# Kernel tuning notes

Hardware: AMD Instinct MI355X
Metric: run time of the kernel (lower is better)

## Reference

```python
import jax, jax.numpy as jnp
import numpy as np

T, BSZ, IDIM, CDIM, NH, N, M = 128, 256, 256, 512, 1, 128, 64


def _address(mem, k, beta, g, s, gamma, w_prev):
    # preproc (matches NTMMemory._preproc)
    beta = jax.nn.softplus(beta)          # [b,1]
    g = jax.nn.sigmoid(g)                 # [b,1]
    s = jax.nn.softmax(s, axis=1)         # [b,3]
    gamma = 1.0 + jax.nn.softplus(gamma)  # [b,1]
    # content addressing: cosine similarity (eps=1e-8 norm clamp as in torch)
    mm = mem + 1e-16                      # [b,N,M]
    kk = k[:, None, :] + 1e-16            # [b,1,M]
    dot = jnp.sum(mm * kk, axis=-1)       # [b,N]
    nm = jnp.maximum(jnp.linalg.norm(mm, axis=-1), 1e-8)
    nk = jnp.maximum(jnp.linalg.norm(kk, axis=-1), 1e-8)
    wc = jax.nn.softmax(beta * (dot / (nm * nk)), axis=1)
    # interpolate
    wg = g * wc + (1.0 - g) * w_prev
    # circular 3-tap shift (modulo convolve): out[i] = s0*w[i-1] + s1*w[i] + s2*w[i+1]
    ww = (s[:, 0:1] * jnp.roll(wg, 1, axis=1)
          + s[:, 1:2] * wg
          + s[:, 2:3] * jnp.roll(wg, -1, axis=1))
    # sharpen
    w = ww ** gamma
    return w / (jnp.sum(w, axis=1, keepdims=True) + 1e-16)


def _split_head(o, m):
    return (o[:, :m], o[:, m:m + 1], o[:, m + 1:m + 2], o[:, m + 2:m + 5], o[:, m + 5:m + 6])


def _forward(inp, hid, c0, mem_bias, r0, W_ih, W_hh, b_ih, b_hh, read_W, read_b, write_W, write_b):
    Tt, bsz, _ = inp.shape
    num_heads = read_W.shape[0]
    n, m = mem_bias.shape
    cdim = c0.shape[0]

    h = hid[0]                                              # [b, cdim]
    c = jnp.broadcast_to(c0, (bsz, cdim))
    mem = jnp.broadcast_to(mem_bias, (bsz, n, m))           # [b, N, M]
    reads = jnp.broadcast_to(r0[:, None, :], (num_heads, bsz, m))
    w_states = jnp.zeros((2 * num_heads, bsz, n), inp.dtype)

    def step(carry, emb):
        h, c, mem, reads, w_states = carry
        x = jnp.concatenate([emb] + [reads[i] for i in range(num_heads)], axis=1)
        gates = x @ W_ih.T + h @ W_hh.T + b_ih + b_hh
        gi, gf, gg, go = jnp.split(gates, 4, axis=1)
        c = jax.nn.sigmoid(gf) * c + jax.nn.sigmoid(gi) * jnp.tanh(gg)
        h = jax.nn.sigmoid(go) * jnp.tanh(c)
        new_reads, new_ws = [], []
        for hi in range(num_heads):
            # read head
            o = h @ read_W[hi] + read_b[hi]                 # [b, M+6]
            k, beta, g, s, gamma = _split_head(o, m)
            w = _address(mem, k, beta, g, s, gamma, w_states[2 * hi])
            new_reads.append(jnp.einsum('bn,bnm->bm', w, mem))
            new_ws.append(w)
            # write head
            o = h @ write_W[hi] + write_b[hi]               # [b, 3M+6]
            k, beta, g, s, gamma = _split_head(o, m)
            e = jax.nn.sigmoid(o[:, m + 6:2 * m + 6])
            a = o[:, 2 * m + 6:3 * m + 6]
            w = _address(mem, k, beta, g, s, gamma, w_states[2 * hi + 1])
            mem = mem * (1.0 - w[:, :, None] * e[:, None, :]) + w[:, :, None] * a[:, None, :]
            new_ws.append(w)
        reads = jnp.stack(new_reads)
        w_states = jnp.stack(new_ws)
        out = jnp.concatenate([h] + new_reads, axis=1)      # [b, cdim + NH*M]
        return (h, c, mem, reads, w_states), out

    _, os = jax.lax.scan(step, (h, c, mem, reads, w_states), inp)
    return os                                               # [T, b, cdim + NH*M]


def setup_inputs() -> dict:
    key = jax.random.key(0)
    ks = jax.random.split(key, 10)
    lstm_std = 5.0 / np.sqrt(IDIM + M * NH + CDIM)
    mem_std = 1.0 / np.sqrt(N + M)
    return {
        'inp': jax.random.normal(ks[0], (T, BSZ, IDIM), jnp.float32),
        'hid': jax.random.normal(ks[1], (1, BSZ, CDIM), jnp.float32) * 0.05,
        'c0': jax.random.normal(ks[2], (CDIM,), jnp.float32) * 0.05,
        'mem_bias': jax.random.uniform(ks[3], (N, M), jnp.float32, -mem_std, mem_std),
        'r0': jax.random.normal(ks[4], (NH, M), jnp.float32) * 0.02,
        'W_ih': jax.random.uniform(ks[5], (4 * CDIM, IDIM + M * NH), jnp.float32, -lstm_std, lstm_std),
        'W_hh': jax.random.uniform(ks[6], (4 * CDIM, CDIM), jnp.float32, -lstm_std, lstm_std),
        'b_ih': jnp.zeros((4 * CDIM,), jnp.float32),
        'b_hh': jnp.zeros((4 * CDIM,), jnp.float32),
        'read_W': jax.random.normal(ks[7], (NH, CDIM, M + 6), jnp.float32) * 0.05,
        'read_b': jnp.zeros((NH, M + 6), jnp.float32),
        'write_W': jax.random.normal(ks[8], (NH, CDIM, 3 * M + 6), jnp.float32) * 0.05,
        'write_b': jnp.zeros((NH, 3 * M + 6), jnp.float32),
    }


def reference(inp, hid, c0, mem_bias, r0, W_ih, W_hh, b_ih, b_hh, read_W, read_b, write_W, write_b):
    return _forward(inp, hid, c0, mem_bias, r0, W_ih, W_hh, b_ih, b_hh,
                    read_W, read_b, write_W, write_b)
```

## Files before the change

kernel.cpp:

```cpp
#include <hip/hip_runtime.h>
#include <math.h>

#define TT   128
#define BSZ  256
#define IDIM 256
#define CDIM 512
#define NN   128
#define MM   64
#define KTOT 832
#define GJ   2048
#define ODIM 576
#define OC   268

#define NKB1 26
#define NJT1 32
#define NKB2 16
#define NJT2 17

typedef __attribute__((ext_vector_type(8))) short s16x8;
typedef __attribute__((ext_vector_type(4))) float f32x4;
#define MFMA __builtin_amdgcn_mfma_f32_16x16x32_bf16

__device__ __forceinline__ float sigmoidf_(float x) { return 1.0f / (1.0f + expf(-x)); }
__device__ __forceinline__ float softplusf_(float x) {
    return (x > 0.f) ? (x + log1pf(expf(-x))) : log1pf(expf(x));
}
__device__ __forceinline__ unsigned short f2bf(float f) {
    unsigned int u = __builtin_bit_cast(unsigned int, f);
    u += 0x7FFFu + ((u >> 16) & 1u);
    return (unsigned short)(u >> 16);
}
__device__ __forceinline__ float bf2f(unsigned short b) {
    unsigned int u = ((unsigned int)b) << 16;
    return __builtin_bit_cast(float, u);
}
__device__ __forceinline__ void split2(float v, unsigned short& h, unsigned short& lo) {
    h = f2bf(v);
    lo = f2bf(v - bf2f(h));
}

__global__ void k_packB1(const float* __restrict__ W_ih, const float* __restrict__ W_hh,
                         const float* __restrict__ b_ih, const float* __restrict__ b_hh,
                         unsigned short* __restrict__ Bh, unsigned short* __restrict__ Bl,
                         float* __restrict__ bias)
{
    const int total = NKB1 * NJT1 * 4 * 64 * 8;
    for (int idx = blockIdx.x * 256 + threadIdx.x; idx < total + GJ; idx += gridDim.x * 256) {
        if (idx < total) {
            int e  = idx & 7;
            int l  = (idx >> 3) & 63;
            int g  = (idx >> 9) & 3;
            int jt = (idx >> 11) & 31;
            int kb = idx >> 16;
            int k  = kb * 32 + ((l >> 4) << 3) + e;
            int n  = g * 512 + jt * 16 + (l & 15);
            float v = (k < 320) ? W_ih[n * 320 + k] : W_hh[n * 512 + (k - 320)];
            unsigned short h_, l_;
            split2(v, h_, l_);
            Bh[idx] = h_; Bl[idx] = l_;
        } else {
            int j = idx - total;
            bias[j] = b_ih[j] + b_hh[j];
        }
    }
}

__global__ void k_packB2(const float* __restrict__ rW, const float* __restrict__ rb,
                         const float* __restrict__ wW, const float* __restrict__ wb,
                         unsigned short* __restrict__ Bh, unsigned short* __restrict__ Bl,
                         float* __restrict__ bias2)
{
    const int total = NKB2 * NJT2 * 64 * 8;
    for (int idx = blockIdx.x * 256 + threadIdx.x; idx < total + NJT2 * 16; idx += gridDim.x * 256) {
        if (idx < total) {
            int e   = idx & 7;
            int l   = (idx >> 3) & 63;
            int q   = idx >> 9;
            int jt  = q % 17;
            int kb  = q / 17;
            int k   = kb * 32 + ((l >> 4) << 3) + e;
            int col = jt * 16 + (l & 15);
            float v = 0.f;
            if (col < 70)       v = rW[k * 70 + col];
            else if (col < OC)  v = wW[k * 198 + (col - 70)];
            unsigned short h_, l_;
            split2(v, h_, l_);
            Bh[idx] = h_; Bl[idx] = l_;
        } else {
            int col = idx - total;
            bias2[col] = (col < 70) ? rb[col] : ((col < OC) ? wb[col - 70] : 0.f);
        }
    }
}

__global__ void k_init(const float* __restrict__ hid, const float* __restrict__ c0,
                       const float* __restrict__ mem_bias, const float* __restrict__ r0,
                       float* __restrict__ h0, float* __restrict__ cst, float* __restrict__ mem,
                       float* __restrict__ rdv, float* __restrict__ w_r, float* __restrict__ w_w)
{
    const int A = BSZ * CDIM;
    const int B = A + BSZ * CDIM;
    const int C = B + BSZ * NN * MM;
    const int D = C + BSZ * MM;
    const int E = D + 2 * BSZ * NN;
    for (int idx = blockIdx.x * 256 + threadIdx.x; idx < E; idx += gridDim.x * 256) {
        if (idx < A) h0[idx] = hid[idx];
        else if (idx < B) { int i = idx - A; cst[i] = c0[i & (CDIM - 1)]; }
        else if (idx < C) { int i = idx - B; mem[i] = mem_bias[i & (NN * MM - 1)]; }
        else if (idx < D) { int i = idx - C; rdv[i] = r0[i & (MM - 1)]; }
        else { int i = idx - D; if (i < BSZ * NN) w_r[i] = 0.f; else w_w[i - BSZ * NN] = 0.f; }
    }
}

__global__ __launch_bounds__(256) void k_gates_mfma(
    const float* __restrict__ x_emb, const float* __restrict__ read_v,
    const float* __restrict__ h_in,
    const unsigned short* __restrict__ Bh, const unsigned short* __restrict__ Bl,
    const float* __restrict__ bias,
    float* __restrict__ c_st, float* __restrict__ h_out, float* __restrict__ out_t)
{
    __shared__ __align__(16) unsigned short AH[4][32][40];
    __shared__ __align__(16) unsigned short AL[4][32][40];
    __shared__ float red[4][32][4][16];
    const int tid = threadIdx.x;
    const int w = tid >> 6, l = tid & 63;
    const int jt = blockIdx.x;
    const int m0 = blockIdx.y * 32;

    f32x4 acc[2][4];
#pragma unroll
    for (int s = 0; s < 2; ++s)
#pragma unroll
        for (int g = 0; g < 4; ++g) acc[s][g] = (f32x4){0.f, 0.f, 0.f, 0.f};

    const int row_s = l >> 1;
    const int c0 = (l & 1) * 16;
    const int rr = l & 15;
    const int kq = (l >> 4) * 8;

    for (int i = 0; i < 7; ++i) {
        const int kb = i * 4 + w;
        const bool act = (kb < NKB1);
        s16x8 bfh[4], bfl[4];
        if (act) {
            const int boff = ((kb * 32 + jt) * 256 + l) * 8;
#pragma unroll
            for (int g = 0; g < 4; ++g) {
                bfh[g] = *(const s16x8*)(Bh + boff + g * 512);
                bfl[g] = *(const s16x8*)(Bl + boff + g * 512);
            }
            const int kg = kb * 32;
            const float* p;
            if (kb < 8)       p = x_emb + (m0 + row_s) * IDIM + kg + c0;
            else if (kb < 10) p = read_v + (m0 + row_s) * MM + (kg - IDIM) + c0;
            else              p = h_in + (m0 + row_s) * CDIM + (kg - 320) + c0;
            float f[16];
            *(float4*)&f[0]  = ((const float4*)p)[0];
            *(float4*)&f[4]  = ((const float4*)p)[1];
            *(float4*)&f[8]  = ((const float4*)p)[2];
            *(float4*)&f[12] = ((const float4*)p)[3];
            s16x8 vh0, vl0, vh1, vl1;
#pragma unroll
            for (int q = 0; q < 8; ++q) {
                unsigned short h_, l_;
                split2(f[q], h_, l_);
                vh0[q] = (short)h_; vl0[q] = (short)l_;
                split2(f[8 + q], h_, l_);
                vh1[q] = (short)h_; vl1[q] = (short)l_;
            }
            *(s16x8*)&AH[w][row_s][c0]     = vh0;
            *(s16x8*)&AH[w][row_s][c0 + 8] = vh1;
            *(s16x8*)&AL[w][row_s][c0]     = vl0;
            *(s16x8*)&AL[w][row_s][c0 + 8] = vl1;
        }
        __syncthreads();
        if (act) {
            s16x8 a0h = *(const s16x8*)&AH[w][rr][kq];
            s16x8 a0l = *(const s16x8*)&AL[w][rr][kq];
            s16x8 a1h = *(const s16x8*)&AH[w][16 + rr][kq];
            s16x8 a1l = *(const s16x8*)&AL[w][16 + rr][kq];
#pragma unroll
            for (int g = 0; g < 4; ++g) {
                acc[0][g] = MFMA(a0h, bfh[g], acc[0][g], 0, 0, 0);
                acc[1][g] = MFMA(a1h, bfh[g], acc[1][g], 0, 0, 0);
                acc[0][g] = MFMA(a0l, bfh[g], acc[0][g], 0, 0, 0);
                acc[1][g] = MFMA(a1l, bfh[g], acc[1][g], 0, 0, 0);
                acc[0][g] = MFMA(a0h, bfl[g], acc[0][g], 0, 0, 0);
                acc[1][g] = MFMA(a1h, bfl[g], acc[1][g], 0, 0, 0);
            }
        }
        __syncthreads();
    }

#pragma unroll
    for (int s = 0; s < 2; ++s)
#pragma unroll
        for (int g = 0; g < 4; ++g)
#pragma unroll
            for (int r = 0; r < 4; ++r)
                red[w][s * 16 + (l >> 4) * 4 + r][g][l & 15] = acc[s][g][r];
    __syncthreads();
    const int j = tid & 15, r0 = tid >> 4;
#pragma unroll
    for (int s = 0; s < 2; ++s) {
        const int row = s * 16 + r0;
        const int b = m0 + row;
        const int jg = jt * 16 + j;
        float gv0 = red[0][row][0][j] + red[1][row][0][j] + red[2][row][0][j] + red[3][row][0][j];
        float gv1 = red[0][row][1][j] + red[1][row][1][j] + red[2][row][1][j] + red[3][row][1][j];
        float gv2 = red[0][row][2][j] + red[1][row][2][j] + red[2][row][2][j] + red[3][row][2][j];
        float gv3 = red[0][row][3][j] + red[1][row][3][j] + red[2][row][3][j] + red[3][row][3][j];
        float gi = gv0 + bias[jg];
        float gf = gv1 + bias[512 + jg];
        float gg = gv2 + bias[1024 + jg];
        float go = gv3 + bias[1536 + jg];
        float cn = sigmoidf_(gf) * c_st[b * CDIM + jg] + sigmoidf_(gi) * tanhf(gg);
        float hn = sigmoidf_(go) * tanhf(cn);
        c_st[b * CDIM + jg] = cn;
        h_out[b * CDIM + jg] = hn;
        out_t[b * ODIM + jg] = hn;
    }
}

__global__ __launch_bounds__(256) void k_heads_mfma(
    const float* __restrict__ h,
    const unsigned short* __restrict__ Bh, const unsigned short* __restrict__ Bl,
    const float* __restrict__ bias2, float* __restrict__ o_all)
{
    __shared__ __align__(16) unsigned short AH[4][16][40];
    __shared__ __align__(16) unsigned short AL[4][16][40];
    __shared__ float red[4][16][16];
    const int tid = threadIdx.x;
    const int w = tid >> 6, l = tid & 63;
    const int jt = blockIdx.x;
    const int m0 = blockIdx.y * 16;

    f32x4 acc = (f32x4){0.f, 0.f, 0.f, 0.f};
    const int row_s = l >> 2;
    const int c0 = (l & 3) * 8;
    const int rr = l & 15;
    const int kq = (l >> 4) * 8;

    for (int i = 0; i < 4; ++i) {
        const int kb = i * 4 + w;
        const int boff = ((kb * NJT2 + jt) * 64 + l) * 8;
        s16x8 bh = *(const s16x8*)(Bh + boff);
        s16x8 bl = *(const s16x8*)(Bl + boff);
        const float* p = h + (m0 + row_s) * CDIM + kb * 32 + c0;
        float f[8];
        *(float4*)&f[0] = ((const float4*)p)[0];
        *(float4*)&f[4] = ((const float4*)p)[1];
        s16x8 vh, vl;
#pragma unroll
        for (int q = 0; q < 8; ++q) {
            unsigned short h_, l_;
            split2(f[q], h_, l_);
            vh[q] = (short)h_; vl[q] = (short)l_;
        }
        *(s16x8*)&AH[w][row_s][c0] = vh;
        *(s16x8*)&AL[w][row_s][c0] = vl;
        __syncthreads();
        s16x8 ah = *(const s16x8*)&AH[w][rr][kq];
        s16x8 al = *(const s16x8*)&AL[w][rr][kq];
        acc = MFMA(ah, bh, acc, 0, 0, 0);
        acc = MFMA(al, bh, acc, 0, 0, 0);
        acc = MFMA(ah, bl, acc, 0, 0, 0);
        __syncthreads();
    }
#pragma unroll
    for (int r = 0; r < 4; ++r)
        red[w][(l >> 4) * 4 + r][l & 15] = acc[r];
    __syncthreads();
    const int j = tid & 15, row = tid >> 4;
    const int col = jt * 16 + j;
    if (col < OC) {
        float o = red[0][row][j] + red[1][row][j] + red[2][row][j] + red[3][row][j] + bias2[col];
        o_all[(m0 + row) * OC + col] = o;
    }
}

__global__ __launch_bounds__(256) void k_address(
    const float* __restrict__ o_all,
    float* __restrict__ mem,
    float* __restrict__ rdv,
    float* __restrict__ w_r,
    float* __restrict__ w_w,
    float* __restrict__ out_t)
{
    const int b = blockIdx.x, tid = threadIdx.x;
    __shared__ float ms[NN * 65];
    __shared__ float os[OC];
    __shared__ float wgs[NN];
    __shared__ float wsh[NN];
    __shared__ float red4[4];
    __shared__ float esh[MM], ash[MM];

    for (int i = tid; i < NN * MM / 4; i += 256) {
        int n = i >> 4, m4 = (i & 15) * 4;
        float4 v = *(const float4*)&mem[(size_t)b * NN * MM + n * MM + m4];
        ms[n * 65 + m4 + 0] = v.x;
        ms[n * 65 + m4 + 1] = v.y;
        ms[n * 65 + m4 + 2] = v.z;
        ms[n * 65 + m4 + 3] = v.w;
    }
    for (int i = tid; i < OC; i += 256) os[i] = o_all[b * OC + i];
    __syncthreads();

    for (int head = 0; head < 2; ++head) {
        const int ob = head ? 70 : 0;
        const float* wprev = head ? w_w : w_r;
        float* wstore = head ? w_w : w_r;

        float beta  = softplusf_(os[ob + 64]);
        float g     = sigmoidf_(os[ob + 65]);
        float s0r = os[ob + 66], s1r = os[ob + 67], s2r = os[ob + 68];
        float smx = fmaxf(s0r, fmaxf(s1r, s2r));
        float e0 = expf(s0r - smx), e1 = expf(s1r - smx), e2 = expf(s2r - smx);
        float einv = 1.f / (e0 + e1 + e2);
        float s0 = e0 * einv, s1 = e1 * einv, s2 = e2 * einv;
        float gamma = 1.f + softplusf_(os[ob + 69]);

        float simv = -1e30f;
        if (tid < NN) {
            float dot = 0.f, nm2 = 0.f, nk2 = 0.f;
            const float* mrow = ms + tid * 65;
#pragma unroll 8
            for (int m = 0; m < MM; ++m) {
                float mv = mrow[m] + 1e-16f;
                float kv = os[ob + m] + 1e-16f;
                dot += mv * kv; nm2 += mv * mv; nk2 += kv * kv;
            }
            float nm = fmaxf(sqrtf(nm2), 1e-8f);
            float nk = fmaxf(sqrtf(nk2), 1e-8f);
            simv = beta * dot / (nm * nk);
        }
        float v = simv;
#pragma unroll
        for (int off = 32; off; off >>= 1) v = fmaxf(v, __shfl_xor(v, off));
        if ((tid & 63) == 0) red4[tid >> 6] = v;
        __syncthreads();
        float smax = fmaxf(fmaxf(red4[0], red4[1]), fmaxf(red4[2], red4[3]));
        __syncthreads();

        float pv = (tid < NN) ? expf(simv - smax) : 0.f;
        v = pv;
#pragma unroll
        for (int off = 32; off; off >>= 1) v += __shfl_xor(v, off);
        if ((tid & 63) == 0) red4[tid >> 6] = v;
        __syncthreads();
        float psum = red4[0] + red4[1] + red4[2] + red4[3];
        __syncthreads();

        if (tid < NN) {
            float wc = pv / psum;
            wgs[tid] = g * wc + (1.f - g) * wprev[b * NN + tid];
        }
        __syncthreads();

        float wv_ = 0.f;
        if (tid < NN) {
            int nl = (tid + NN - 1) & (NN - 1), nr = (tid + 1) & (NN - 1);
            float wwv = s0 * wgs[nl] + s1 * wgs[tid] + s2 * wgs[nr];
            wv_ = powf(wwv, gamma);
        }
        v = wv_;
#pragma unroll
        for (int off = 32; off; off >>= 1) v += __shfl_xor(v, off);
        if ((tid & 63) == 0) red4[tid >> 6] = v;
        __syncthreads();
        float wsum = red4[0] + red4[1] + red4[2] + red4[3];
        __syncthreads();

        if (tid < NN) {
            float wfin = wv_ / (wsum + 1e-16f);
            wsh[tid] = wfin;
            wstore[b * NN + tid] = wfin;
        }
        __syncthreads();

        if (head == 0) {
            if (tid < MM) {
                float r = 0.f;
#pragma unroll 8
                for (int n = 0; n < NN; ++n) r += wsh[n] * ms[n * 65 + tid];
                rdv[b * MM + tid] = r;
                out_t[b * ODIM + CDIM + tid] = r;
            }
            __syncthreads();
        } else {
            if (tid < MM) {
                esh[tid] = sigmoidf_(os[140 + tid]);
                ash[tid] = os[204 + tid];
            }
            __syncthreads();
            for (int i = tid; i < NN * MM / 4; i += 256) {
                int n = i >> 4, m4 = (i & 15) * 4;
                float wvn = wsh[n];
                float4 r;
                r.x = ms[n * 65 + m4 + 0] * (1.f - wvn * esh[m4 + 0]) + wvn * ash[m4 + 0];
                r.y = ms[n * 65 + m4 + 1] * (1.f - wvn * esh[m4 + 1]) + wvn * ash[m4 + 1];
                r.z = ms[n * 65 + m4 + 2] * (1.f - wvn * esh[m4 + 2]) + wvn * ash[m4 + 2];
                r.w = ms[n * 65 + m4 + 3] * (1.f - wvn * esh[m4 + 3]) + wvn * ash[m4 + 3];
                *(float4*)&mem[(size_t)b * NN * MM + n * MM + m4] = r;
            }
            __syncthreads();
        }
    }
}

extern "C" void kernel_launch(void* const* d_in, const int* in_sizes, int n_in,
                              void* d_out, int out_size, void* d_ws, size_t ws_size,
                              hipStream_t stream) {
    const float* inp      = (const float*)d_in[0];
    const float* hid      = (const float*)d_in[1];
    const float* c0       = (const float*)d_in[2];
    const float* mem_bias = (const float*)d_in[3];
    const float* r0       = (const float*)d_in[4];
    const float* W_ih     = (const float*)d_in[5];
    const float* W_hh     = (const float*)d_in[6];
    const float* b_ih     = (const float*)d_in[7];
    const float* b_hh     = (const float*)d_in[8];
    const float* read_W   = (const float*)d_in[9];
    const float* read_b   = (const float*)d_in[10];
    const float* write_W  = (const float*)d_in[11];
    const float* write_b  = (const float*)d_in[12];
    float* out = (float*)d_out;

    char* p = (char*)d_ws;
    auto alloc = [&](size_t bytes) { char* r = p; p += (bytes + 255) & ~(size_t)255; return r; };
    const size_t nB1 = (size_t)NKB1 * NJT1 * 4 * 64 * 8;
    const size_t nB2 = (size_t)NKB2 * NJT2 * 64 * 8;
    unsigned short* B1h = (unsigned short*)alloc(nB1 * 2);
    unsigned short* B1l = (unsigned short*)alloc(nB1 * 2);
    unsigned short* B2h = (unsigned short*)alloc(nB2 * 2);
    unsigned short* B2l = (unsigned short*)alloc(nB2 * 2);
    float* bias1 = (float*)alloc(GJ * 4);
    float* bias2 = (float*)alloc(NJT2 * 16 * 4);
    float* h0    = (float*)alloc((size_t)BSZ * CDIM * 4);
    float* h1    = (float*)alloc((size_t)BSZ * CDIM * 4);
    float* cst   = (float*)alloc((size_t)BSZ * CDIM * 4);
    float* mem   = (float*)alloc((size_t)BSZ * NN * MM * 4);
    float* rdv   = (float*)alloc((size_t)BSZ * MM * 4);
    float* w_r   = (float*)alloc((size_t)BSZ * NN * 4);
    float* w_w   = (float*)alloc((size_t)BSZ * NN * 4);
    float* o_all = (float*)alloc((size_t)BSZ * OC * 4);

    k_packB1<<<4096, 256, 0, stream>>>(W_ih, W_hh, b_ih, b_hh, B1h, B1l, bias1);
    k_packB2<<<600, 256, 0, stream>>>(read_W, read_b, write_W, write_b, B2h, B2l, bias2);
    k_init<<<2048, 256, 0, stream>>>(hid, c0, mem_bias, r0, h0, cst, mem, rdv, w_r, w_w);

    for (int t = 0; t < TT; ++t) {
        const float* hin = (t & 1) ? h1 : h0;
        float* hout      = (t & 1) ? h0 : h1;
        float* out_t = out + (size_t)t * BSZ * ODIM;
        k_gates_mfma<<<dim3(NJT1, 8), 256, 0, stream>>>(
            inp + (size_t)t * BSZ * IDIM, rdv, hin, B1h, B1l, bias1, cst, hout, out_t);
        k_heads_mfma<<<dim3(NJT2, 16), 256, 0, stream>>>(
            hout, B2h, B2l, bias2, o_all);
        k_address<<<BSZ, 256, 0, stream>>>(o_all, mem, rdv, w_r, w_w, out_t);
    }
}
```

Before: 3.867 ms.

## Fuse per-timestep kernels into one persistent kernel with grid barriers

Replaces the three kernels launched per timestep (gates, heads, addressing) with a single persistent kernel of 256 blocks that loops over all timesteps and separates phases with a custom hierarchical atomic grid barrier. Each block keeps its batch row's memory matrix, read/write weights and LSTM cell state in shared memory or registers across timesteps, so the per-step global round-trips of memory and state go away. This is meant to remove about 384 kernel launches and the global memory traffic for state, at the cost of spin-wait barriers, reliance on all 256 blocks being co-resident, and heavier shared memory use per block.

```diff
diff --git a/kernel.cpp b/kernel.cpp
--- a/kernel.cpp
+++ b/kernel.cpp
@@ -16,33 +16,34 @@
 #define NJT1 32
 #define NKB2 16
 #define NJT2 17
+#define NBLK 256
 
 typedef __attribute__((ext_vector_type(8))) short s16x8;
 typedef __attribute__((ext_vector_type(4))) float f32x4;
+typedef unsigned short ush;
 #define MFMA __builtin_amdgcn_mfma_f32_16x16x32_bf16
 
 __device__ __forceinline__ float sigmoidf_(float x) { return 1.0f / (1.0f + expf(-x)); }
 __device__ __forceinline__ float softplusf_(float x) {
     return (x > 0.f) ? (x + log1pf(expf(-x))) : log1pf(expf(x));
 }
-__device__ __forceinline__ unsigned short f2bf(float f) {
+__device__ __forceinline__ ush f2bf(float f) {
     unsigned int u = __builtin_bit_cast(unsigned int, f);
     u += 0x7FFFu + ((u >> 16) & 1u);
-    return (unsigned short)(u >> 16);
-}
-__device__ __forceinline__ float bf2f(unsigned short b) {
+    return (ush)(u >> 16);
+}
+__device__ __forceinline__ float bf2f(ush b) {
     unsigned int u = ((unsigned int)b) << 16;
     return __builtin_bit_cast(float, u);
 }
-__device__ __forceinline__ void split2(float v, unsigned short& h, unsigned short& lo) {
+__device__ __forceinline__ void split2(float v, ush& h, ush& lo) {
     h = f2bf(v);
     lo = f2bf(v - bf2f(h));
 }
 
 __global__ void k_packB1(const float* __restrict__ W_ih, const float* __restrict__ W_hh,
                          const float* __restrict__ b_ih, const float* __restrict__ b_hh,
-                         unsigned short* __restrict__ Bh, unsigned short* __restrict__ Bl,
-                         float* __restrict__ bias)
+                         ush* __restrict__ Bh, ush* __restrict__ Bl, float* __restrict__ bias)
 {
     const int total = NKB1 * NJT1 * 4 * 64 * 8;
     for (int idx = blockIdx.x * 256 + threadIdx.x; idx < total + GJ; idx += gridDim.x * 256) {
@@ -55,7 +56,7 @@
             int k  = kb * 32 + ((l >> 4) << 3) + e;
             int n  = g * 512 + jt * 16 + (l & 15);
             float v = (k < 320) ? W_ih[n * 320 + k] : W_hh[n * 512 + (k - 320)];
-            unsigned short h_, l_;
+            ush h_, l_;
             split2(v, h_, l_);
             Bh[idx] = h_; Bl[idx] = l_;
         } else {
@@ -67,8 +68,7 @@
 
 __global__ void k_packB2(const float* __restrict__ rW, const float* __restrict__ rb,
                          const float* __restrict__ wW, const float* __restrict__ wb,
-                         unsigned short* __restrict__ Bh, unsigned short* __restrict__ Bl,
-                         float* __restrict__ bias2)
+                         ush* __restrict__ Bh, ush* __restrict__ Bl, float* __restrict__ bias2)
 {
     const int total = NKB2 * NJT2 * 64 * 8;
     for (int idx = blockIdx.x * 256 + threadIdx.x; idx < total + NJT2 * 16; idx += gridDim.x * 256) {
@@ -83,7 +83,7 @@
             float v = 0.f;
             if (col < 70)       v = rW[k * 70 + col];
             else if (col < OC)  v = wW[k * 198 + (col - 70)];
-            unsigned short h_, l_;
+            ush h_, l_;
             split2(v, h_, l_);
             Bh[idx] = h_; Bl[idx] = l_;
         } else {
@@ -93,318 +93,389 @@
     }
 }
 
-__global__ void k_init(const float* __restrict__ hid, const float* __restrict__ c0,
-                       const float* __restrict__ mem_bias, const float* __restrict__ r0,
-                       float* __restrict__ h0, float* __restrict__ cst, float* __restrict__ mem,
-                       float* __restrict__ rdv, float* __restrict__ w_r, float* __restrict__ w_w)
+__global__ void k_barinit(unsigned* __restrict__ bar) {
+    for (int i = threadIdx.x; i < 160; i += 64) bar[i] = 0u;
+}
+
+__device__ __forceinline__ void gridbar(unsigned* bar, int bid) {
+    __syncthreads();
+    if (threadIdx.x == 0) {
+        __threadfence();
+        unsigned g = __hip_atomic_load(&bar[144], __ATOMIC_RELAXED, __HIP_MEMORY_SCOPE_AGENT);
+        int grp = bid >> 5;
+        unsigned old = __hip_atomic_fetch_add(&bar[grp * 16], 1u, __ATOMIC_ACQ_REL, __HIP_MEMORY_SCOPE_AGENT);
+        if (old == 31u) {
+            unsigned r = __hip_atomic_fetch_add(&bar[128], 1u, __ATOMIC_ACQ_REL, __HIP_MEMORY_SCOPE_AGENT);
+            if (r == 7u) {
+                __hip_atomic_store(&bar[128], 0u, __ATOMIC_RELAXED, __HIP_MEMORY_SCOPE_AGENT);
+                for (int i = 0; i < 8; ++i)
+                    __hip_atomic_store(&bar[i * 16], 0u, __ATOMIC_RELAXED, __HIP_MEMORY_SCOPE_AGENT);
+                __hip_atomic_store(&bar[144], g + 1u, __ATOMIC_RELEASE, __HIP_MEMORY_SCOPE_AGENT);
+            } else {
+                while (__hip_atomic_load(&bar[144], __ATOMIC_ACQUIRE, __HIP_MEMORY_SCOPE_AGENT) == g)
+                    __builtin_amdgcn_s_sleep(2);
+            }
+        } else {
+            while (__hip_atomic_load(&bar[144], __ATOMIC_ACQUIRE, __HIP_MEMORY_SCOPE_AGENT) == g)
+                __builtin_amdgcn_s_sleep(2);
+        }
+        __threadfence();
+    }
+    __syncthreads();
+}
+
+__global__ __launch_bounds__(256, 2) void k_persist(
+    const float* __restrict__ inp,
+    const float* __restrict__ hid, const float* __restrict__ c0,
+    const float* __restrict__ mem_bias, const float* __restrict__ r0,
+    const ush* __restrict__ B1h, const ush* __restrict__ B1l, const float* __restrict__ bias1,
+    const ush* __restrict__ B2h, const ush* __restrict__ B2l, const float* __restrict__ bias2,
+    float* __restrict__ h0, float* __restrict__ h1,
+    float* __restrict__ rdv, float* __restrict__ o_all,
+    float* __restrict__ out, unsigned* __restrict__ bar)
 {
-    const int A = BSZ * CDIM;
-    const int B = A + BSZ * CDIM;
-    const int C = B + BSZ * NN * MM;
-    const int D = C + BSZ * MM;
-    const int E = D + 2 * BSZ * NN;
-    for (int idx = blockIdx.x * 256 + threadIdx.x; idx < E; idx += gridDim.x * 256) {
-        if (idx < A) h0[idx] = hid[idx];
-        else if (idx < B) { int i = idx - A; cst[i] = c0[i & (CDIM - 1)]; }
-        else if (idx < C) { int i = idx - B; mem[i] = mem_bias[i & (NN * MM - 1)]; }
-        else if (idx < D) { int i = idx - C; rdv[i] = r0[i & (MM - 1)]; }
-        else { int i = idx - D; if (i < BSZ * NN) w_r[i] = 0.f; else w_w[i - BSZ * NN] = 0.f; }
-    }
-}
-
-__global__ __launch_bounds__(256) void k_gates_mfma(
-    const float* __restrict__ x_emb, const float* __restrict__ read_v,
-    const float* __restrict__ h_in,
-    const unsigned short* __restrict__ Bh, const unsigned short* __restrict__ Bl,
-    const float* __restrict__ bias,
-    float* __restrict__ c_st, float* __restrict__ h_out, float* __restrict__ out_t)
-{
-    __shared__ __align__(16) unsigned short AH[4][32][40];
-    __shared__ __align__(16) unsigned short AL[4][32][40];
-    __shared__ float red[4][32][4][16];
+    __shared__ __align__(16) char scratch[20480];
+    __shared__ float ms[NN * 65];
+    __shared__ float wr_s[NN], ww_s[NN];
+    __shared__ float os[OC];
+    __shared__ float wgs[NN], wsh[NN];
+    __shared__ float red4[4];
+    __shared__ float esh[MM], ash[MM];
+
+    const int bid = blockIdx.x;
     const int tid = threadIdx.x;
-    const int w = tid >> 6, l = tid & 63;
-    const int jt = blockIdx.x;
-    const int m0 = blockIdx.y * 32;
-
-    f32x4 acc[2][4];
-#pragma unroll
-    for (int s = 0; s < 2; ++s)
-#pragma unroll
-        for (int g = 0; g < 4; ++g) acc[s][g] = (f32x4){0.f, 0.f, 0.f, 0.f};
-
-    const int row_s = l >> 1;
-    const int c0 = (l & 1) * 16;
+    const int wid = tid >> 6, l = tid & 63;
     const int rr = l & 15;
     const int kq = (l >> 4) * 8;
 
-    for (int i = 0; i < 7; ++i) {
-        const int kb = i * 4 + w;
-        const bool act = (kb < NKB1);
-        s16x8 bfh[4], bfl[4];
-        if (act) {
-            const int boff = ((kb * 32 + jt) * 256 + l) * 8;
-#pragma unroll
-            for (int g = 0; g < 4; ++g) {
-                bfh[g] = *(const s16x8*)(Bh + boff + g * 512);
-                bfl[g] = *(const s16x8*)(Bl + boff + g * 512);
-            }
-            const int kg = kb * 32;
-            const float* p;
-            if (kb < 8)       p = x_emb + (m0 + row_s) * IDIM + kg + c0;
-            else if (kb < 10) p = read_v + (m0 + row_s) * MM + (kg - IDIM) + c0;
-            else              p = h_in + (m0 + row_s) * CDIM + (kg - 320) + c0;
-            float f[16];
-            *(float4*)&f[0]  = ((const float4*)p)[0];
-            *(float4*)&f[4]  = ((const float4*)p)[1];
-            *(float4*)&f[8]  = ((const float4*)p)[2];
-            *(float4*)&f[12] = ((const float4*)p)[3];
-            s16x8 vh0, vl0, vh1, vl1;
-#pragma unroll
-            for (int q = 0; q < 8; ++q) {
-                unsigned short h_, l_;
-                split2(f[q], h_, l_);
-                vh0[q] = (short)h_; vl0[q] = (short)l_;
-                split2(f[8 + q], h_, l_);
-                vh1[q] = (short)h_; vl1[q] = (short)l_;
-            }
-            *(s16x8*)&AH[w][row_s][c0]     = vh0;
-            *(s16x8*)&AH[w][row_s][c0 + 8] = vh1;
-            *(s16x8*)&AL[w][row_s][c0]     = vl0;
-            *(s16x8*)&AL[w][row_s][c0 + 8] = vl1;
+    ush (*AH)[32][40] = (ush (*)[32][40])scratch;
+    ush (*AL)[32][40] = (ush (*)[32][40])(scratch + 10240);
+
+    for (int i = tid; i < NN * MM; i += 256) {
+        int n = i >> 6, m = i & 63;
+        ms[n * 65 + m] = mem_bias[i];
+    }
+    if (tid < NN) { wr_s[tid] = 0.f; ww_s[tid] = 0.f; }
+    for (int k = tid; k < CDIM; k += 256) h0[bid * CDIM + k] = hid[bid * CDIM + k];
+    if (tid < MM) rdv[bid * MM + tid] = r0[tid];
+
+    const int jt = bid & 31;
+    const int m0 = (bid >> 5) * 32;
+    float c_reg[2][4];
+    float bjv[4];
+    {
+        int jg = jt * 16 + rr;
+#pragma unroll
+        for (int s = 0; s < 2; ++s)
+#pragma unroll
+            for (int r = 0; r < 4; ++r) c_reg[s][r] = c0[jg];
+        bjv[0] = bias1[jg];        bjv[1] = bias1[512 + jg];
+        bjv[2] = bias1[1024 + jg]; bjv[3] = bias1[1536 + jg];
+    }
+    const int jt2 = bid % 17, mt2 = bid / 17;
+    const int mm0 = mt2 * 32;
+    const int col2 = jt2 * 16 + (tid & 15);
+    float b2v = (col2 < OC) ? bias2[col2] : 0.f;
+
+    gridbar(bar, bid);
+
+    for (int t = 0; t < TT; ++t) {
+        const float* hin = (t & 1) ? h1 : h0;
+        float* hout      = (t & 1) ? h0 : h1;
+        float* out_t = out + (size_t)t * BSZ * ODIM;
+
+        {
+            const float* x_t = inp + (size_t)t * BSZ * IDIM;
+            f32x4 acc[2][4];
+#pragma unroll
+            for (int s = 0; s < 2; ++s)
+#pragma unroll
+                for (int g = 0; g < 4; ++g) acc[s][g] = (f32x4){0.f, 0.f, 0.f, 0.f};
+
+            const int row_s = l >> 1;
+            const int cc = (l & 1) * 16;
+
+            for (int i = 0; i < 7; ++i) {
+                const int kb = i * 4 + wid;
+                const bool act = (kb < NKB1);
+                s16x8 bfh[4], bfl[4];
+                if (act) {
+                    const int boff = ((kb * 32 + jt) * 256 + l) * 8;
+#pragma unroll
+                    for (int g = 0; g < 4; ++g) {
+                        bfh[g] = *(const s16x8*)(B1h + boff + g * 512);
+                        bfl[g] = *(const s16x8*)(B1l + boff + g * 512);
+                    }
+                    const int kg = kb * 32;
+                    const float* p;
+                    if (kb < 8)       p = x_t + (m0 + row_s) * IDIM + kg + cc;
+                    else if (kb < 10) p = rdv + (m0 + row_s) * MM + (kg - IDIM) + cc;
+                    else              p = hin + (m0 + row_s) * CDIM + (kg - 320) + cc;
+                    float f[16];
+                    *(float4*)&f[0]  = ((const float4*)p)[0];
+                    *(float4*)&f[4]  = ((const float4*)p)[1];
+                    *(float4*)&f[8]  = ((const float4*)p)[2];
+                    *(float4*)&f[12] = ((const float4*)p)[3];
+                    s16x8 vh0, vl0, vh1, vl1;
+#pragma unroll
+                    for (int q = 0; q < 8; ++q) {
+                        ush h_, l_;
+                        split2(f[q], h_, l_);
+                        vh0[q] = (short)h_; vl0[q] = (short)l_;
+                        split2(f[8 + q], h_, l_);
+                        vh1[q] = (short)h_; vl1[q] = (short)l_;
+                    }
+                    *(s16x8*)&AH[wid][row_s][cc]     = vh0;
+                    *(s16x8*)&AH[wid][row_s][cc + 8] = vh1;
+                    *(s16x8*)&AL[wid][row_s][cc]     = vl0;
+                    *(s16x8*)&AL[wid][row_s][cc + 8] = vl1;
+                }
+                __syncthreads();
+                if (act) {
+                    s16x8 a0h = *(const s16x8*)&AH[wid][rr][kq];
+                    s16x8 a0l = *(const s16x8*)&AL[wid][rr][kq];
+                    s16x8 a1h = *(const s16x8*)&AH[wid][16 + rr][kq];
+                    s16x8 a1l = *(const s16x8*)&AL[wid][16 + rr][kq];
+#pragma unroll
+                    for (int g = 0; g < 4; ++g) {
+                        acc[0][g] = MFMA(a0h, bfh[g], acc[0][g], 0, 0, 0);
+                        acc[1][g] = MFMA(a1h, bfh[g], acc[1][g], 0, 0, 0);
+                        acc[0][g] = MFMA(a0l, bfh[g], acc[0][g], 0, 0, 0);
+                        acc[1][g] = MFMA(a1l, bfh[g], acc[1][g], 0, 0, 0);
+                        acc[0][g] = MFMA(a0h, bfl[g], acc[0][g], 0, 0, 0);
+                        acc[1][g] = MFMA(a1h, bfl[g], acc[1][g], 0, 0, 0);
+                    }
+                }
+                __syncthreads();
+            }
+
+            float* red0 = (float*)scratch;
+            float* red1 = (float*)(scratch + 8192);
+            if (wid >= 2) {
+                float* dst = (wid == 2) ? red0 : red1;
+#pragma unroll
+                for (int s = 0; s < 2; ++s)
+#pragma unroll
+                    for (int g = 0; g < 4; ++g)
+#pragma unroll
+                        for (int r = 0; r < 4; ++r)
+                            dst[((s * 16 + (l >> 4) * 4 + r) << 6) + (g << 4) + rr] = acc[s][g][r];
+            }
+            __syncthreads();
+            if (wid < 2) {
+                const float* src = (wid == 0) ? red0 : red1;
+#pragma unroll
+                for (int s = 0; s < 2; ++s)
+#pragma unroll
+                    for (int g = 0; g < 4; ++g)
+#pragma unroll
+                        for (int r = 0; r < 4; ++r)
+                            acc[s][g][r] += src[((s * 16 + (l >> 4) * 4 + r) << 6) + (g << 4) + rr];
+            }
+            __syncthreads();
+            if (wid == 1) {
+#pragma unroll
+                for (int s = 0; s < 2; ++s)
+#pragma unroll
+                    for (int g = 0; g < 4; ++g)
+#pragma unroll
+                        for (int r = 0; r < 4; ++r)
+                            red0[((s * 16 + (l >> 4) * 4 + r) << 6) + (g << 4) + rr] = acc[s][g][r];
+            }
+            __syncthreads();
+            if (wid == 0) {
+                const int jg = jt * 16 + rr;
+#pragma unroll
+                for (int s = 0; s < 2; ++s)
+#pragma unroll
+                    for (int r = 0; r < 4; ++r) {
+                        const int row = s * 16 + (l >> 4) * 4 + r;
+                        const int ridx = (row << 6) + rr;
+                        float gi = acc[s][0][r] + red0[ridx]        + bjv[0];
+                        float gf = acc[s][1][r] + red0[ridx + 16]   + bjv[1];
+                        float gg2 = acc[s][2][r] + red0[ridx + 32]  + bjv[2];
+                        float go = acc[s][3][r] + red0[ridx + 48]   + bjv[3];
+                        float cn = sigmoidf_(gf) * c_reg[s][r] + sigmoidf_(gi) * tanhf(gg2);
+                        float hn = sigmoidf_(go) * tanhf(cn);
+                        c_reg[s][r] = cn;
+                        const int b = m0 + row;
+                        hout[b * CDIM + jg] = hn;
+                        out_t[b * ODIM + jg] = hn;
+                    }
+            }
         }
-        __syncthreads();
-        if (act) {
-            s16x8 a0h = *(const s16x8*)&AH[w][rr][kq];
-            s16x8 a0l = *(const s16x8*)&AL[w][rr][kq];
-            s16x8 a1h = *(const s16x8*)&AH[w][16 + rr][kq];
-            s16x8 a1l = *(const s16x8*)&AL[w][16 + rr][kq];
-#pragma unroll
-            for (int g = 0; g < 4; ++g) {
-                acc[0][g] = MFMA(a0h, bfh[g], acc[0][g], 0, 0, 0);
-                acc[1][g] = MFMA(a1h, bfh[g], acc[1][g], 0, 0, 0);
-                acc[0][g] = MFMA(a0l, bfh[g], acc[0][g], 0, 0, 0);
-                acc[1][g] = MFMA(a1l, bfh[g], acc[1][g], 0, 0, 0);
-                acc[0][g] = MFMA(a0h, bfl[g], acc[0][g], 0, 0, 0);
-                acc[1][g] = MFMA(a1h, bfl[g], acc[1][g], 0, 0, 0);
+
+        gridbar(bar, bid);
+
+        if (bid < 136) {
+            f32x4 acc2[2];
+            acc2[0] = (f32x4){0.f, 0.f, 0.f, 0.f};
+            acc2[1] = (f32x4){0.f, 0.f, 0.f, 0.f};
+            const int row_s = l >> 1;
+            const int cc = (l & 1) * 16;
+            for (int i = 0; i < 4; ++i) {
+                const int kb = i * 4 + wid;
+                const int boff = ((kb * NJT2 + jt2) * 64 + l) * 8;
+                s16x8 bh = *(const s16x8*)(B2h + boff);
+                s16x8 bl = *(const s16x8*)(B2l + boff);
+                const float* p = hout + (mm0 + row_s) * CDIM + kb * 32 + cc;
+                float f[16];
+                *(float4*)&f[0]  = ((const float4*)p)[0];
+                *(float4*)&f[4]  = ((const float4*)p)[1];
+                *(float4*)&f[8]  = ((const float4*)p)[2];
+                *(float4*)&f[12] = ((const float4*)p)[3];
+                s16x8 vh0, vl0, vh1, vl1;
+#pragma unroll
+                for (int q = 0; q < 8; ++q) {
+                    ush h_, l_;
+                    split2(f[q], h_, l_);
+                    vh0[q] = (short)h_; vl0[q] = (short)l_;
+                    split2(f[8 + q], h_, l_);
+                    vh1[q] = (short)h_; vl1[q] = (short)l_;
+                }
+                *(s16x8*)&AH[wid][row_s][cc]     = vh0;
+                *(s16x8*)&AH[wid][row_s][cc + 8] = vh1;
+                *(s16x8*)&AL[wid][row_s][cc]     = vl0;
+                *(s16x8*)&AL[wid][row_s][cc + 8] = vl1;
+                __syncthreads();
+                s16x8 a0h = *(const s16x8*)&AH[wid][rr][kq];
+                s16x8 a0l = *(const s16x8*)&AL[wid][rr][kq];
+                s16x8 a1h = *(const s16x8*)&AH[wid][16 + rr][kq];
+                s16x8 a1l = *(const s16x8*)&AL[wid][16 + rr][kq];
+                acc2[0] = MFMA(a0h, bh, acc2[0], 0, 0, 0);
+                acc2[1] = MFMA(a1h, bh, acc2[1], 0, 0, 0);
+                acc2[0] = MFMA(a0l, bh, acc2[0], 0, 0, 0);
+                acc2[1] = MFMA(a1l, bh, acc2[1], 0, 0, 0);
+                acc2[0] = MFMA(a0h, bl, acc2[0], 0, 0, 0);
+                acc2[1] = MFMA(a1h, bl, acc2[1], 0, 0, 0);
+                __syncthreads();
+            }
+            float* red2 = (float*)scratch;
+#pragma unroll
+            for (int s = 0; s < 2; ++s)
+#pragma unroll
+                for (int r = 0; r < 4; ++r)
+                    red2[((wid * 32 + s * 16 + (l >> 4) * 4 + r) << 4) + rr] = acc2[s][r];
+            __syncthreads();
+            if (col2 < OC) {
+#pragma unroll
+                for (int s = 0; s < 2; ++s) {
+                    const int row = s * 16 + (tid >> 4);
+                    const int j = tid & 15;
+                    float o = red2[((row) << 4) + j] + red2[((32 + row) << 4) + j]
+                            + red2[((64 + row) << 4) + j] + red2[((96 + row) << 4) + j] + b2v;
+                    o_all[(mm0 + row) * OC + col2] = o;
+                }
             }
         }
-        __syncthreads();
-    }
-
-#pragma unroll
-    for (int s = 0; s < 2; ++s)
-#pragma unroll
-        for (int g = 0; g < 4; ++g)
-#pragma unroll
-            for (int r = 0; r < 4; ++r)
-                red[w][s * 16 + (l >> 4) * 4 + r][g][l & 15] = acc[s][g][r];
-    __syncthreads();
-    const int j = tid & 15, r0 = tid >> 4;
-#pragma unroll
-    for (int s = 0; s < 2; ++s) {
-        const int row = s * 16 + r0;
-        const int b = m0 + row;
-        const int jg = jt * 16 + j;
-        float gv0 = red[0][row][0][j] + red[1][row][0][j] + red[2][row][0][j] + red[3][row][0][j];
-        float gv1 = red[0][row][1][j] + red[1][row][1][j] + red[2][row][1][j] + red[3][row][1][j];
-        float gv2 = red[0][row][2][j] + red[1][row][2][j] + red[2][row][2][j] + red[3][row][2][j];
-        float gv3 = red[0][row][3][j] + red[1][row][3][j] + red[2][row][3][j] + red[3][row][3][j];
-        float gi = gv0 + bias[jg];
-        float gf = gv1 + bias[512 + jg];
-        float gg = gv2 + bias[1024 + jg];
-        float go = gv3 + bias[1536 + jg];
-        float cn = sigmoidf_(gf) * c_st[b * CDIM + jg] + sigmoidf_(gi) * tanhf(gg);
-        float hn = sigmoidf_(go) * tanhf(cn);
-        c_st[b * CDIM + jg] = cn;
-        h_out[b * CDIM + jg] = hn;
-        out_t[b * ODIM + jg] = hn;
-    }
-}
-
-__global__ __launch_bounds__(256) void k_heads_mfma(
-    const float* __restrict__ h,
-    const unsigned short* __restrict__ Bh, const unsigned short* __restrict__ Bl,
-    const float* __restrict__ bias2, float* __restrict__ o_all)
-{
-    __shared__ __align__(16) unsigned short AH[4][16][40];
-    __shared__ __align__(16) unsigned short AL[4][16][40];
-    __shared__ float red[4][16][16];
-    const int tid = threadIdx.x;
-    const int w = tid >> 6, l = tid & 63;
-    const int jt = blockIdx.x;
-    const int m0 = blockIdx.y * 16;
-
-    f32x4 acc = (f32x4){0.f, 0.f, 0.f, 0.f};
-    const int row_s = l >> 2;
-    const int c0 = (l & 3) * 8;
-    const int rr = l & 15;
-    const int kq = (l >> 4) * 8;
-
-    for (int i = 0; i < 4; ++i) {
-        const int kb = i * 4 + w;
-        const int boff = ((kb * NJT2 + jt) * 64 + l) * 8;
-        s16x8 bh = *(const s16x8*)(Bh + boff);
-        s16x8 bl = *(const s16x8*)(Bl + boff);
-        const float* p = h + (m0 + row_s) * CDIM + kb * 32 + c0;
-        float f[8];
-        *(float4*)&f[0] = ((const float4*)p)[0];
-        *(float4*)&f[4] = ((const float4*)p)[1];
-        s16x8 vh, vl;
-#pragma unroll
-        for (int q = 0; q < 8; ++q) {
-            unsigned short h_, l_;
-            split2(f[q], h_, l_);
-            vh[q] = (short)h_; vl[q] = (short)l_;
+
+        gridbar(bar, bid);
+
+        {
+            for (int i = tid; i < OC; i += 256) os[i] = o_all[bid * OC + i];
+            __syncthreads();
+
+            for (int head = 0; head < 2; ++head) {
+                const int ob = head ? 70 : 0;
+                float* wst = head ? ww_s : wr_s;
+
+                float beta = softplusf_(os[ob + 64]);
+                float gte  = sigmoidf_(os[ob + 65]);
+                float s0r = os[ob + 66], s1r = os[ob + 67], s2r = os[ob + 68];
+                float smx = fmaxf(s0r, fmaxf(s1r, s2r));
+                float e0 = expf(s0r - smx), e1 = expf(s1r - smx), e2 = expf(s2r - smx);
+                float einv = 1.f / (e0 + e1 + e2);
+                float s0 = e0 * einv, s1 = e1 * einv, s2 = e2 * einv;
+                float gamma = 1.f + softplusf_(os[ob + 69]);
+
+                float simv = -1e30f;
+                if (tid < NN) {
+                    float dot = 0.f, nm2 = 0.f, nk2 = 0.f;
+                    const float* mrow = ms + tid * 65;
+#pragma unroll 8
+                    for (int m = 0; m < MM; ++m) {
+                        float mv = mrow[m] + 1e-16f;
+                        float kv = os[ob + m] + 1e-16f;
+                        dot += mv * kv; nm2 += mv * mv; nk2 += kv * kv;
+                    }
+                    float nm = fmaxf(sqrtf(nm2), 1e-8f);
+                    float nk = fmaxf(sqrtf(nk2), 1e-8f);
+                    simv = beta * dot / (nm * nk);
+                }
+                float v = simv;
+#pragma unroll
+                for (int off = 32; off; off >>= 1) v = fmaxf(v, __shfl_xor(v, off));
+                if ((tid & 63) == 0) red4[tid >> 6] = v;
+                __syncthreads();
+                float smax = fmaxf(fmaxf(red4[0], red4[1]), fmaxf(red4[2], red4[3]));
+                __syncthreads();
+
+                float pv = (tid < NN) ? expf(simv - smax) : 0.f;
+                v = pv;
+#pragma unroll
+                for (int off = 32; off; off >>= 1) v += __shfl_xor(v, off);
+                if ((tid & 63) == 0) red4[tid >> 6] = v;
+                __syncthreads();
+                float psum = red4[0] + red4[1] + red4[2] + red4[3];
+                __syncthreads();
+
+                if (tid < NN) {
+                    float wc = pv / psum;
+                    wgs[tid] = gte * wc + (1.f - gte) * wst[tid];
+                }
+                __syncthreads();
+
+                float wv_ = 0.f;
+                if (tid < NN) {
+                    int nl = (tid + NN - 1) & (NN - 1), nr = (tid + 1) & (NN - 1);
+                    float wwv = s0 * wgs[nl] + s1 * wgs[tid] + s2 * wgs[nr];
+                    wv_ = powf(wwv, gamma);
+                }
+                v = wv_;
+#pragma unroll
+                for (int off = 32; off; off >>= 1) v += __shfl_xor(v, off);
+                if ((tid & 63) == 0) red4[tid >> 6] = v;
+                __syncthreads();
+                float wsum = red4[0] + red4[1] + red4[2] + red4[3];
+                __syncthreads();
+
+                if (tid < NN) {
+                    float wfin = wv_ / (wsum + 1e-16f);
+                    wsh[tid] = wfin;
+                    wst[tid] = wfin;
+                }
+                __syncthreads();
+
+                if (head == 0) {
+                    if (tid < MM) {
+                        float r = 0.f;
+#pragma unroll 8
+                        for (int n = 0; n < NN; ++n) r += wsh[n] * ms[n * 65 + tid];
+                        rdv[bid * MM + tid] = r;
+                        out_t[bid * ODIM + CDIM + tid] = r;
+                    }
+                    __syncthreads();
+                } else {
+                    if (tid < MM) {
+                        esh[tid] = sigmoidf_(os[140 + tid]);
+                        ash[tid] = os[204 + tid];
+                    }
+                    __syncthreads();
+                    for (int i = tid; i < NN * MM / 4; i += 256) {
+                        int n = i >> 4, m4 = (i & 15) * 4;
+                        float wvn = wsh[n];
+#pragma unroll
+                        for (int q = 0; q < 4; ++q) {
+                            float mv = ms[n * 65 + m4 + q];
+                            ms[n * 65 + m4 + q] = mv * (1.f - wvn * esh[m4 + q]) + wvn * ash[m4 + q];
+                        }
+                    }
+                    __syncthreads();
+                }
+            }
         }
-        *(s16x8*)&AH[w][row_s][c0] = vh;
-        *(s16x8*)&AL[w][row_s][c0] = vl;
-        __syncthreads();
-        s16x8 ah = *(const s16x8*)&AH[w][rr][kq];
-        s16x8 al = *(const s16x8*)&AL[w][rr][kq];
-        acc = MFMA(ah, bh, acc, 0, 0, 0);
-        acc = MFMA(al, bh, acc, 0, 0, 0);
-        acc = MFMA(ah, bl, acc, 0, 0, 0);
-        __syncthreads();
-    }
-#pragma unroll
-    for (int r = 0; r < 4; ++r)
-        red[w][(l >> 4) * 4 + r][l & 15] = acc[r];
-    __syncthreads();
-    const int j = tid & 15, row = tid >> 4;
-    const int col = jt * 16 + j;
-    if (col < OC) {
-        float o = red[0][row][j] + red[1][row][j] + red[2][row][j] + red[3][row][j] + bias2[col];
-        o_all[(m0 + row) * OC + col] = o;
-    }
-}
-
-__global__ __launch_bounds__(256) void k_address(
-    const float* __restrict__ o_all,
-    float* __restrict__ mem,
-    float* __restrict__ rdv,
-    float* __restrict__ w_r,
-    float* __restrict__ w_w,
-    float* __restrict__ out_t)
-{
-    const int b = blockIdx.x, tid = threadIdx.x;
-    __shared__ float ms[NN * 65];
-    __shared__ float os[OC];
-    __shared__ float wgs[NN];
-    __shared__ float wsh[NN];
-    __shared__ float red4[4];
-    __shared__ float esh[MM], ash[MM];
-
-    for (int i = tid; i < NN * MM / 4; i += 256) {
-        int n = i >> 4, m4 = (i & 15) * 4;
-        float4 v = *(const float4*)&mem[(size_t)b * NN * MM + n * MM + m4];
-        ms[n * 65 + m4 + 0] = v.x;
-        ms[n * 65 + m4 + 1] = v.y;
-        ms[n * 65 + m4 + 2] = v.z;
-        ms[n * 65 + m4 + 3] = v.w;
-    }
-    for (int i = tid; i < OC; i += 256) os[i] = o_all[b * OC + i];
-    __syncthreads();
-
-    for (int head = 0; head < 2; ++head) {
-        const int ob = head ? 70 : 0;
-        const float* wprev = head ? w_w : w_r;
-        float* wstore = head ? w_w : w_r;
-
-        float beta  = softplusf_(os[ob + 64]);
-        float g     = sigmoidf_(os[ob + 65]);
-        float s0r = os[ob + 66], s1r = os[ob + 67], s2r = os[ob + 68];
-        float smx = fmaxf(s0r, fmaxf(s1r, s2r));
-        float e0 = expf(s0r - smx), e1 = expf(s1r - smx), e2 = expf(s2r - smx);
-        float einv = 1.f / (e0 + e1 + e2);
-        float s0 = e0 * einv, s1 = e1 * einv, s2 = e2 * einv;
-        float gamma = 1.f + softplusf_(os[ob + 69]);
-
-        float simv = -1e30f;
-        if (tid < NN) {
-            float dot = 0.f, nm2 = 0.f, nk2 = 0.f;
-            const float* mrow = ms + tid * 65;
-#pragma unroll 8
-            for (int m = 0; m < MM; ++m) {
-                float mv = mrow[m] + 1e-16f;
-                float kv = os[ob + m] + 1e-16f;
-                dot += mv * kv; nm2 += mv * mv; nk2 += kv * kv;
-            }
-            float nm = fmaxf(sqrtf(nm2), 1e-8f);
-            float nk = fmaxf(sqrtf(nk2), 1e-8f);
-            simv = beta * dot / (nm * nk);
-        }
-        float v = simv;
-#pragma unroll
-        for (int off = 32; off; off >>= 1) v = fmaxf(v, __shfl_xor(v, off));
-        if ((tid & 63) == 0) red4[tid >> 6] = v;
-        __syncthreads();
-        float smax = fmaxf(fmaxf(red4[0], red4[1]), fmaxf(red4[2], red4[3]));
-        __syncthreads();
-
-        float pv = (tid < NN) ? expf(simv - smax) : 0.f;
-        v = pv;
-#pragma unroll
-        for (int off = 32; off; off >>= 1) v += __shfl_xor(v, off);
-        if ((tid & 63) == 0) red4[tid >> 6] = v;
-        __syncthreads();
-        float psum = red4[0] + red4[1] + red4[2] + red4[3];
-        __syncthreads();
-
-        if (tid < NN) {
-            float wc = pv / psum;
-            wgs[tid] = g * wc + (1.f - g) * wprev[b * NN + tid];
-        }
-        __syncthreads();
-
-        float wv_ = 0.f;
-        if (tid < NN) {
-            int nl = (tid + NN - 1) & (NN - 1), nr = (tid + 1) & (NN - 1);
-            float wwv = s0 * wgs[nl] + s1 * wgs[tid] + s2 * wgs[nr];
-            wv_ = powf(wwv, gamma);
-        }
-        v = wv_;
-#pragma unroll
-        for (int off = 32; off; off >>= 1) v += __shfl_xor(v, off);
-        if ((tid & 63) == 0) red4[tid >> 6] = v;
-        __syncthreads();
-        float wsum = red4[0] + red4[1] + red4[2] + red4[3];
-        __syncthreads();
-
-        if (tid < NN) {
-            float wfin = wv_ / (wsum + 1e-16f);
-            wsh[tid] = wfin;
-            wstore[b * NN + tid] = wfin;
-        }
-        __syncthreads();
-
-        if (head == 0) {
-            if (tid < MM) {
-                float r = 0.f;
-#pragma unroll 8
-                for (int n = 0; n < NN; ++n) r += wsh[n] * ms[n * 65 + tid];
-                rdv[b * MM + tid] = r;
-                out_t[b * ODIM + CDIM + tid] = r;
-            }
-            __syncthreads();
-        } else {
-            if (tid < MM) {
-                esh[tid] = sigmoidf_(os[140 + tid]);
-                ash[tid] = os[204 + tid];
-            }
-            __syncthreads();
-            for (int i = tid; i < NN * MM / 4; i += 256) {
-                int n = i >> 4, m4 = (i & 15) * 4;
-                float wvn = wsh[n];
-                float4 r;
-                r.x = ms[n * 65 + m4 + 0] * (1.f - wvn * esh[m4 + 0]) + wvn * ash[m4 + 0];
-                r.y = ms[n * 65 + m4 + 1] * (1.f - wvn * esh[m4 + 1]) + wvn * ash[m4 + 1];
-                r.z = ms[n * 65 + m4 + 2] * (1.f - wvn * esh[m4 + 2]) + wvn * ash[m4 + 2];
-                r.w = ms[n * 65 + m4 + 3] * (1.f - wvn * esh[m4 + 3]) + wvn * ash[m4 + 3];
-                *(float4*)&mem[(size_t)b * NN * MM + n * MM + m4] = r;
-            }
-            __syncthreads();
-        }
+
+        gridbar(bar, bid);
     }
 }
 
@@ -430,33 +501,24 @@
     auto alloc = [&](size_t bytes) { char* r = p; p += (bytes + 255) & ~(size_t)255; return r; };
     const size_t nB1 = (size_t)NKB1 * NJT1 * 4 * 64 * 8;
     const size_t nB2 = (size_t)NKB2 * NJT2 * 64 * 8;
-    unsigned short* B1h = (unsigned short*)alloc(nB1 * 2);
-    unsigned short* B1l = (unsigned short*)alloc(nB1 * 2);
-    unsigned short* B2h = (unsigned short*)alloc(nB2 * 2);
-    unsigned short* B2l = (unsigned short*)alloc(nB2 * 2);
+    ush* B1h = (ush*)alloc(nB1 * 2);
+    ush* B1l = (ush*)alloc(nB1 * 2);
+    ush* B2h = (ush*)alloc(nB2 * 2);
+    ush* B2l = (ush*)alloc(nB2 * 2);
     float* bias1 = (float*)alloc(GJ * 4);
     float* bias2 = (float*)alloc(NJT2 * 16 * 4);
     float* h0    = (float*)alloc((size_t)BSZ * CDIM * 4);
     float* h1    = (float*)alloc((size_t)BSZ * CDIM * 4);
-    float* cst   = (float*)alloc((size_t)BSZ * CDIM * 4);
-    float* mem   = (float*)alloc((size_t)BSZ * NN * MM * 4);
     float* rdv   = (float*)alloc((size_t)BSZ * MM * 4);
-    float* w_r   = (float*)alloc((size_t)BSZ * NN * 4);
-    float* w_w   = (float*)alloc((size_t)BSZ * NN * 4);
     float* o_all = (float*)alloc((size_t)BSZ * OC * 4);
-
-    k_packB1<<<4096, 256, 0, stream>>>(W_ih, W_hh, b_ih, b_hh, B1h, B1l, bias1);
-    k_packB2<<<600, 256, 0, stream>>>(read_W, read_b, write_W, write_b, B2h, B2l, bias2);
-    k_init<<<2048, 256, 0, stream>>>(hid, c0, mem_bias, r0, h0, cst, mem, rdv, w_r, w_w);
-
-    for (int t = 0; t < TT; ++t) {
-        const float* hin = (t & 1) ? h1 : h0;
-        float* hout      = (t & 1) ? h0 : h1;
-        float* out_t = out + (size_t)t * BSZ * ODIM;
-        k_gates_mfma<<<dim3(NJT1, 8), 256, 0, stream>>>(
-            inp + (size_t)t * BSZ * IDIM, rdv, hin, B1h, B1l, bias1, cst, hout, out_t);
-        k_heads_mfma<<<dim3(NJT2, 16), 256, 0, stream>>>(
-            hout, B2h, B2l, bias2, o_all);
-        k_address<<<BSZ, 256, 0, stream>>>(o_all, mem, rdv, w_r, w_w, out_t);
-    }
-}
+    unsigned* bar = (unsigned*)alloc(256 * 4);
+
+    k_packB1<<<2048, 256, 0, stream>>>(W_ih, W_hh, b_ih, b_hh, B1h, B1l, bias1);
+    k_packB2<<<544, 256, 0, stream>>>(read_W, read_b, write_W, write_b, B2h, B2l, bias2);
+    k_barinit<<<1, 64, 0, stream>>>(bar);
+
+    k_persist<<<dim3(NBLK), dim3(256), 0, stream>>>(
+        inp, hid, c0, mem_bias, r0,
+        B1h, B1l, bias1, B2h, B2l, bias2,
+        h0, h1, rdv, o_all, out, bar);
+}
```

Result: slower. 14.12 ms (+265.2%).
